# Optimization experiments

Measured on AMD Instinct MI355X. Metric: run time of the kernel, lower is better.

## Reference

```python
import jax, jax.numpy as jnp
import numpy as np

NUM_GRAPHS = 512


def setup_inputs() -> dict:
    key = jax.random.key(0)
    ks = jax.random.split(key, 12)
    N, F = 100000, 9
    E = 1600000
    x = jax.random.normal(ks[0], (N, F), dtype=jnp.float32)
    edge_index = jax.random.randint(ks[1], (2, E), 0, N, dtype=jnp.int64)
    batch = jnp.sort(jax.random.randint(ks[2], (N,), 0, NUM_GRAPHS, dtype=jnp.int64))
    def lin(k, fan_in, fan_out):
        k1, k2 = jax.random.split(k)
        bound = 1.0 / np.sqrt(fan_in)
        W = jax.random.uniform(k1, (fan_out, fan_in), jnp.float32, -bound, bound)
        b = jax.random.uniform(k2, (fan_out,), jnp.float32, -bound, bound)
        return W, b
    W1, b1 = lin(ks[3], F, 64)
    W2, b2 = lin(ks[4], 64, 128)
    W3, b3 = lin(ks[5], 128, 64)
    Wfc, bfc = lin(ks[6], 64, 11)
    return {"x": x, "edge_index": edge_index, "batch": batch,
            "W1": W1, "b1": b1, "W2": W2, "b2": b2,
            "W3": W3, "b3": b3, "Wfc": Wfc, "bfc": bfc}


def reference(x, edge_index, batch, W1, b1, W2, b2, W3, b3, Wfc, bfc):
    N = x.shape[0]
    src, dst = edge_index[0], edge_index[1]

    def gin_layer(h, W, b):
        # GINConv (eps=0): Lin((1+eps)*h_i + sum_{j->i} h_j), then relu
        agg = jax.ops.segment_sum(h[src], dst, num_segments=N)
        return jax.nn.relu((h + agg) @ W.T + b)

    h = gin_layer(x, W1, b1)   # [N, 64]
    h = gin_layer(h, W2, b2)   # [N, 128]
    h = gin_layer(h, W3, b3)   # [N, 64]

    # global_mean_pool over graph ids
    sums = jax.ops.segment_sum(h, batch, num_segments=NUM_GRAPHS)           # [G, 64]
    counts = jax.ops.segment_sum(jnp.ones((N,), h.dtype), batch,
                                 num_segments=NUM_GRAPHS)                   # [G]
    pooled = sums / jnp.maximum(counts, 1.0)[:, None]
    return pooled @ Wfc.T + bfc  # [G, num_classes]
```

## Files before the change

### kernel.cpp

```cpp
#include <hip/hip_runtime.h>
#include <hip/hip_bf16.h>


#define NBLK 256
#define CFBS 512
#define RB   128
#define NBMAX 1024
#define SCBS 1024

__device__ inline float bf2f(unsigned short u) {
    return __uint_as_float((unsigned)u << 16);
}
__device__ inline unsigned short f2bf(float f) {
    unsigned x = __float_as_uint(f);
    return (unsigned short)((x + 0x7FFFu + ((x >> 16) & 1u)) >> 16);
}
__device__ inline float lo16(unsigned u) { return __uint_as_float(u << 16); }
__device__ inline float hi16(unsigned u) { return __uint_as_float(u & 0xFFFF0000u); }


__global__ __launch_bounds__(CFBS) void count_kernel(
    const int* __restrict__ dst, int* __restrict__ cnt, int E, int NB)
{
    __shared__ int hist[NBMAX];
    int tid = threadIdx.x;
    for (int i = tid; i < NBMAX; i += CFBS) hist[i] = 0;
    __syncthreads();
    for (int e = blockIdx.x * CFBS + tid; e < E; e += NBLK * CFBS)
        atomicAdd(&hist[dst[e] >> 7], 1);
    __syncthreads();
    for (int b = tid; b < NB; b += CFBS)
        cnt[b * NBLK + blockIdx.x] = hist[b];
}

__global__ __launch_bounds__(SCBS) void scan_k1(
    const int* __restrict__ cnt, int* __restrict__ ofs,
    int* __restrict__ part, int NT)
{
    __shared__ int tmp[SCBS];
    int i = blockIdx.x * SCBS + threadIdx.x;
    int v = (i < NT) ? cnt[i] : 0;
    tmp[threadIdx.x] = v;
    __syncthreads();
    for (int off = 1; off < SCBS; off <<= 1) {
        int t = (threadIdx.x >= off) ? tmp[threadIdx.x - off] : 0;
        __syncthreads();
        tmp[threadIdx.x] += t;
        __syncthreads();
    }
    if (i < NT) ofs[i] = tmp[threadIdx.x] - v;
    if (threadIdx.x == SCBS - 1) part[blockIdx.x] = tmp[threadIdx.x];
}

__global__ __launch_bounds__(SCBS) void scan_k2(int* __restrict__ part, int B)
{
    __shared__ int tmp[SCBS];
    int v = (threadIdx.x < B) ? part[threadIdx.x] : 0;
    tmp[threadIdx.x] = v;
    __syncthreads();
    for (int off = 1; off < SCBS; off <<= 1) {
        int t = (threadIdx.x >= off) ? tmp[threadIdx.x - off] : 0;
        __syncthreads();
        tmp[threadIdx.x] += t;
        __syncthreads();
    }
    if (threadIdx.x < B) part[threadIdx.x] = tmp[threadIdx.x] - v;
}

__global__ __launch_bounds__(SCBS) void scan_k3(
    int* __restrict__ ofs, const int* __restrict__ part, int NT)
{
    int i = blockIdx.x * SCBS + threadIdx.x;
    if (i < NT) ofs[i] += part[blockIdx.x];
}

__global__ __launch_bounds__(CFBS) void fillp_kernel(
    const int* __restrict__ src, const int* __restrict__ dst,
    const int* __restrict__ ofs, int* __restrict__ pairs, int E, int NB)
{
    __shared__ int cur[NBMAX];
    int tid = threadIdx.x;
    for (int b = tid; b < NB; b += CFBS)
        cur[b] = ofs[b * NBLK + blockIdx.x];
    __syncthreads();
    for (int e = blockIdx.x * CFBS + tid; e < E; e += NBLK * CFBS) {
        int d = dst[e];
        int b = d >> 7, dl = d & 127;
        int pos = atomicAdd(&cur[b], 1);
        pairs[pos] = (dl << 20) | src[e];
    }
}

__global__ __launch_bounds__(512) void bucket_csr_kernel(
    const int* __restrict__ pairs, const int* __restrict__ ofs,
    int* __restrict__ rowstart, int* __restrict__ eidx, int N, int E, int NB)
{
    __shared__ int deg[RB], pfx[RB], cur[RB];
    int tid = threadIdx.x;
    int b = blockIdx.x, n0 = b << 7;
    int e0 = ofs[b * NBLK];
    int e1 = (b + 1 < NB) ? ofs[(b + 1) * NBLK] : E;
    if (tid < RB) deg[tid] = 0;
    __syncthreads();
    for (int e = e0 + tid; e < e1; e += 512)
        atomicAdd(&deg[pairs[e] >> 20], 1);
    __syncthreads();
    if (tid < RB) pfx[tid] = deg[tid];
    __syncthreads();
    for (int off = 1; off < RB; off <<= 1) {
        int t = (tid < RB && tid >= off) ? pfx[tid - off] : 0;
        __syncthreads();
        if (tid < RB) pfx[tid] += t;
        __syncthreads();
    }
    if (tid < RB) {
        int ex = pfx[tid] - deg[tid];
        cur[tid] = ex;
        int n = n0 + tid;
        if (n < N) rowstart[n] = e0 + ex;
    }
    if (b == NB - 1 && tid == 0) rowstart[N] = E;
    __syncthreads();
    for (int e = e0 + tid; e < e1; e += 512) {
        int p = pairs[e];
        int pos = e0 + atomicAdd(&cur[p >> 20], 1);
        eidx[pos] = p & 0xFFFFF;
    }
}


__global__ __launch_bounds__(256) void xprep_kernel(
    const float* __restrict__ x, unsigned short* __restrict__ xb, int N)
{
    int n = blockIdx.x * 256 + threadIdx.x;
    if (n >= N) return;
    unsigned short r[16];
    #pragma unroll
    for (int k = 0; k < 9; ++k) r[k] = f2bf(x[(size_t)n * 9 + k]);
    #pragma unroll
    for (int k = 9; k < 16; ++k) r[k] = 0;
    uint4 u0, u1;
    u0.x = r[0] | ((unsigned)r[1] << 16);  u0.y = r[2] | ((unsigned)r[3] << 16);
    u0.z = r[4] | ((unsigned)r[5] << 16);  u0.w = r[6] | ((unsigned)r[7] << 16);
    u1.x = r[8] | ((unsigned)r[9] << 16);  u1.y = 0; u1.z = 0; u1.w = 0;
    *(uint4*)&xb[(size_t)n * 16]     = u0;
    *(uint4*)&xb[(size_t)n * 16 + 8] = u1;
}


__global__ __launch_bounds__(256) void node1v_kernel(
    const unsigned short* __restrict__ xb, const int* __restrict__ rs,
    const int* __restrict__ eidx, const float* __restrict__ W1,
    const float* __restrict__ b1, unsigned short* __restrict__ h1, int N)
{
    __shared__ float Wl[576];
    __shared__ float bl[64];
    for (int i = threadIdx.x; i < 576; i += 256) Wl[i] = W1[i];
    if (threadIdx.x < 64) bl[threadIdx.x] = b1[threadIdx.x];
    __syncthreads();
    int wid = threadIdx.x >> 6;
    int lane = threadIdx.x & 63;
    int g  = lane >> 2;
    int d4 = lane & 3;
    int nb = blockIdx.x * 16 + wid * 4;
    if (nb >= N) return;

    int n[4], e0[4], dg[4];
    float A0[4], A1[4], A2[4], A3[4];
    #pragma unroll
    for (int i = 0; i < 4; ++i) {
        n[i] = min(nb + i, N - 1);
        e0[i] = rs[n[i]];
        dg[i] = rs[n[i] + 1] - e0[i];
        A0[i] = A1[i] = A2[i] = A3[i] = 0.f;
    }
    #pragma unroll
    for (int i = 0; i < 4; ++i) {
        if (g == 0) {
            uint2 u = *(const uint2*)&xb[(size_t)n[i] * 16 + d4 * 4];
            A0[i] += lo16(u.x); A1[i] += hi16(u.x);
            A2[i] += lo16(u.y); A3[i] += hi16(u.y);
        }
    }
    int mdeg = max(max(dg[0], dg[1]), max(dg[2], dg[3]));
    for (int w0 = 0; w0 < mdeg; w0 += 64) {
        int sidx[4], wd[4];
        #pragma unroll
        for (int i = 0; i < 4; ++i) {
            wd[i] = min(max(dg[i] - w0, 0), 64);
            sidx[i] = (lane < wd[i]) ? eidx[e0[i] + w0 + lane] : 0;
        }
        int mwd = max(max(wd[0], wd[1]), max(wd[2], wd[3]));
        for (int c = 0; c < mwd; c += 16) {
            #pragma unroll
            for (int i = 0; i < 4; ++i) {
                int idx = c + g;
                int s = __shfl(sidx[i], idx < wd[i] ? idx : 0);
                float m = (idx < wd[i]) ? 1.f : 0.f;
                uint2 u = *(const uint2*)&xb[(size_t)s * 16 + d4 * 4];
                A0[i] += m * lo16(u.x); A1[i] += m * hi16(u.x);
                A2[i] += m * lo16(u.y); A3[i] += m * hi16(u.y);
            }
        }
    }
    #pragma unroll
    for (int m = 4; m < 64; m <<= 1) {
        #pragma unroll
        for (int i = 0; i < 4; ++i) {
            A0[i] += __shfl_xor(A0[i], m); A1[i] += __shfl_xor(A1[i], m);
            A2[i] += __shfl_xor(A2[i], m); A3[i] += __shfl_xor(A3[i], m);
        }
    }
    const float* wr = &Wl[lane * 9];
    #pragma unroll
    for (int i = 0; i < 4; ++i) {
        float xv0 = __shfl(A0[i], 0), xv1 = __shfl(A1[i], 0);
        float xv2 = __shfl(A2[i], 0), xv3 = __shfl(A3[i], 0);
        float xv4 = __shfl(A0[i], 1), xv5 = __shfl(A1[i], 1);
        float xv6 = __shfl(A2[i], 1), xv7 = __shfl(A3[i], 1);
        float xv8 = __shfl(A0[i], 2);
        float s = bl[lane] + xv0 * wr[0] + xv1 * wr[1] + xv2 * wr[2]
                + xv3 * wr[3] + xv4 * wr[4] + xv5 * wr[5] + xv6 * wr[6]
                + xv7 * wr[7] + xv8 * wr[8];
        if (nb + i < N)
            h1[(size_t)(nb + i) * 64 + lane] = f2bf(fmaxf(s, 0.f));
    }
}


template<bool BIAS_RELU>
__global__ __launch_bounds__(256) void gather64v_kernel(
    const unsigned short* __restrict__ feat, const int* __restrict__ rs,
    const int* __restrict__ eidx, const float* __restrict__ bias,
    unsigned short* __restrict__ out, int N)
{
    int wid = threadIdx.x >> 6;
    int lane = threadIdx.x & 63;
    int g  = lane >> 4;
    int d4 = lane & 15;
    int nb = blockIdx.x * 16 + wid * 4;
    if (nb >= N) return;

    int n[4], e0[4], dg[4];
    float A0[4], A1[4], A2[4], A3[4];
    #pragma unroll
    for (int i = 0; i < 4; ++i) {
        n[i] = min(nb + i, N - 1);
        e0[i] = rs[n[i]];
        dg[i] = rs[n[i] + 1] - e0[i];
        A0[i] = A1[i] = A2[i] = A3[i] = 0.f;
    }
    #pragma unroll
    for (int i = 0; i < 4; ++i) {
        if (g == 0) {
            uint2 u = *(const uint2*)&feat[(size_t)n[i] * 64 + d4 * 4];
            A0[i] += lo16(u.x); A1[i] += hi16(u.x);
            A2[i] += lo16(u.y); A3[i] += hi16(u.y);
        }
    }
    int mdeg = max(max(dg[0], dg[1]), max(dg[2], dg[3]));
    for (int w0 = 0; w0 < mdeg; w0 += 64) {
        int sidx[4], wd[4];
        #pragma unroll
        for (int i = 0; i < 4; ++i) {
            wd[i] = min(max(dg[i] - w0, 0), 64);
            sidx[i] = (lane < wd[i]) ? eidx[e0[i] + w0 + lane] : 0;
        }
        int mwd = max(max(wd[0], wd[1]), max(wd[2], wd[3]));
        for (int c = 0; c < mwd; c += 8) {
            #pragma unroll
            for (int i = 0; i < 4; ++i) {
                int i0 = c + g, i1 = c + 4 + g;
                int s0 = __shfl(sidx[i], i0 < wd[i] ? i0 : 0);
                int s1 = __shfl(sidx[i], i1 < wd[i] ? i1 : 0);
                float m0 = (i0 < wd[i]) ? 1.f : 0.f;
                float m1 = (i1 < wd[i]) ? 1.f : 0.f;
                uint2 u0 = *(const uint2*)&feat[(size_t)s0 * 64 + d4 * 4];
                uint2 u1 = *(const uint2*)&feat[(size_t)s1 * 64 + d4 * 4];
                A0[i] += m0 * lo16(u0.x) + m1 * lo16(u1.x);
                A1[i] += m0 * hi16(u0.x) + m1 * hi16(u1.x);
                A2[i] += m0 * lo16(u0.y) + m1 * lo16(u1.y);
                A3[i] += m0 * hi16(u0.y) + m1 * hi16(u1.y);
            }
        }
    }
    #pragma unroll
    for (int m = 16; m < 64; m <<= 1) {
        #pragma unroll
        for (int i = 0; i < 4; ++i) {
            A0[i] += __shfl_xor(A0[i], m); A1[i] += __shfl_xor(A1[i], m);
            A2[i] += __shfl_xor(A2[i], m); A3[i] += __shfl_xor(A3[i], m);
        }
    }
    float4 bv = make_float4(0.f, 0.f, 0.f, 0.f);
    if (BIAS_RELU) bv = *(const float4*)&bias[d4 * 4];
    #pragma unroll
    for (int i = 0; i < 4; ++i) {
        if (g == 0 && nb + i < N) {
            float a0 = A0[i], a1 = A1[i], a2 = A2[i], a3 = A3[i];
            if (BIAS_RELU) {
                a0 = fmaxf(a0 + bv.x, 0.f); a1 = fmaxf(a1 + bv.y, 0.f);
                a2 = fmaxf(a2 + bv.z, 0.f); a3 = fmaxf(a3 + bv.w, 0.f);
            }
            ushort4 u;
            u.x = f2bf(a0); u.y = f2bf(a1); u.z = f2bf(a2); u.w = f2bf(a3);
            *(ushort4*)&out[(size_t)(nb + i) * 64 + d4 * 4] = u;
        }
    }
}


template<int IN, int OUT, bool RELU>
__global__ __launch_bounds__(256) void linear_mfma_kernel(
    const unsigned short* __restrict__ A, const float* __restrict__ W,
    const float* __restrict__ bias, unsigned short* __restrict__ Y, int N)
{
    using s8v = __attribute__((ext_vector_type(8))) short;
    using f4v = __attribute__((ext_vector_type(4))) float;
    constexpr int KT = IN / 32;
    constexpr int CT = OUT / 16;
    constexpr int INP = IN + 8;
    __shared__ __align__(16) unsigned short Wb[OUT * INP];
    __shared__ float bl[OUT];
    int tid = threadIdx.x;
    for (int i = tid; i < OUT * IN; i += 256) {
        int o = i / IN, k = i % IN;
        Wb[o * INP + k] = f2bf(W[i]);
    }
    for (int i = tid; i < OUT; i += 256) bl[i] = bias ? bias[i] : 0.f;
    __syncthreads();

    int w = tid >> 6, lane = tid & 63;
    int n0 = blockIdx.x * 64 + w * 16;
    int hl = lane >> 4;
    int ll = lane & 15;

    int an = n0 + ll;
    if (an >= N) an = N - 1;
    const unsigned short* arow = &A[(size_t)an * IN + hl * 8];
    s8v a[KT];
    #pragma unroll
    for (int ks = 0; ks < KT; ++ks) a[ks] = *(const s8v*)&arow[ks * 32];

    f4v acc[CT];
    #pragma unroll
    for (int c = 0; c < CT; ++c) acc[c] = (f4v){0.f, 0.f, 0.f, 0.f};
    #pragma unroll
    for (int c = 0; c < CT; ++c) {
        const unsigned short* wrow = &Wb[(c * 16 + ll) * INP + hl * 8];
        #pragma unroll
        for (int ks = 0; ks < KT; ++ks) {
            s8v b = *(const s8v*)&wrow[ks * 32];
            acc[c] = __builtin_amdgcn_mfma_f32_16x16x32_bf16(a[ks], b, acc[c], 0, 0, 0);
        }
    }
    #pragma unroll
    for (int c = 0; c < CT; ++c) {
        int col = c * 16 + ll;
        float bv = bl[col];
        #pragma unroll
        for (int r = 0; r < 4; ++r) {
            int gn = n0 + hl * 4 + r;
            if (gn < N) {
                float v = acc[c][r] + bv;
                if (RELU) v = fmaxf(v, 0.f);
                Y[(size_t)gn * OUT + col] = f2bf(v);
            }
        }
    }
}


__device__ inline int lower_bound_i(const int* a, int n, int v) {
    int lo = 0, hi = n;
    while (lo < hi) {
        int mid = (lo + hi) >> 1;
        if (a[mid] < v) lo = mid + 1; else hi = mid;
    }
    return lo;
}

__global__ __launch_bounds__(256) void pool_fc_kernel(
    const unsigned short* __restrict__ h3, const int* __restrict__ batch,
    const float* __restrict__ Wfc, const float* __restrict__ bfc,
    float* __restrict__ out, int N)
{
    int g = blockIdx.x;
    int tid = threadIdx.x;
    int w = tid >> 6, lane = tid & 63;
    int lo = lower_bound_i(batch, N, g);
    int hi = lower_bound_i(batch, N, g + 1);
    float sum = 0.f;
    for (int i = lo + w; i < hi; i += 4)
        sum += bf2f(h3[(size_t)i * 64 + lane]);
    __shared__ float P[4][64];
    P[w][lane] = sum;
    __syncthreads();
    if (w == 0) {
        float s = P[0][lane] + P[1][lane] + P[2][lane] + P[3][lane];
        float cnt = (float)((hi - lo) > 0 ? (hi - lo) : 1);
        P[0][lane] = s / cnt;
    }
    __syncthreads();
    if (tid < 11) {
        float s = bfc[tid];
        const float* wr = &Wfc[tid * 64];
        #pragma unroll 8
        for (int k = 0; k < 64; ++k) s += P[0][k] * wr[k];
        out[g * 11 + tid] = s;
    }
}


extern "C" void kernel_launch(void* const* d_in, const int* in_sizes, int n_in,
                              void* d_out, int out_size, void* d_ws, size_t ws_size,
                              hipStream_t stream) {
    const float* x    = (const float*)d_in[0];
    const int*   ei   = (const int*)d_in[1];
    const int*   batch= (const int*)d_in[2];
    const float* W1   = (const float*)d_in[3];
    const float* b1   = (const float*)d_in[4];
    const float* W2   = (const float*)d_in[5];
    const float* b2   = (const float*)d_in[6];
    const float* W3   = (const float*)d_in[7];
    const float* b3   = (const float*)d_in[8];
    const float* Wfc  = (const float*)d_in[9];
    const float* bfc  = (const float*)d_in[10];
    float* out = (float*)d_out;

    const int N = in_sizes[2];
    const int E = in_sizes[1] / 2;
    const int G = out_size / 11;
    const int* src = ei;
    const int* dst = ei + E;
    const int NB = (N + RB - 1) / RB;
    const int NT = NB * NBLK;
    const int SB = (NT + SCBS - 1) / SCBS;

    unsigned short* B1 = (unsigned short*)d_ws;
    unsigned short* B2 = B1 + (size_t)64 * N;
    unsigned short* B3 = B2 + (size_t)64 * N;
    unsigned short* XB = B3 + (size_t)128 * N;
    int* pairs    = (int*)(XB + (size_t)16 * N);
    int* eidx     = pairs + E;
    int* rowstart = eidx + E;
    int* cnt      = rowstart + (N + 1);
    int* ofs      = cnt + NT;
    int* part     = ofs + NT;

    unsigned short* h1   = B1;
    unsigned short* buf2 = B2;
    unsigned short* h2   = B3;
    unsigned short* t3   = B1;
    unsigned short* h3   = B2;
    unsigned short* xb   = XB;

    count_kernel<<<NBLK, CFBS, 0, stream>>>(dst, cnt, E, NB);
    scan_k1<<<SB, SCBS, 0, stream>>>(cnt, ofs, part, NT);
    scan_k2<<<1, SCBS, 0, stream>>>(part, SB);
    scan_k3<<<SB, SCBS, 0, stream>>>(ofs, part, NT);
    fillp_kernel<<<NBLK, CFBS, 0, stream>>>(src, dst, ofs, pairs, E, NB);
    bucket_csr_kernel<<<NB, 512, 0, stream>>>(pairs, ofs, rowstart, eidx, N, E, NB);
    xprep_kernel<<<(N + 255) / 256, 256, 0, stream>>>(x, xb, N);

    node1v_kernel<<<(N + 15) / 16, 256, 0, stream>>>(
        xb, rowstart, eidx, W1, b1, h1, N);

    gather64v_kernel<false><<<(N + 15) / 16, 256, 0, stream>>>(
        h1, rowstart, eidx, nullptr, buf2, N);
    linear_mfma_kernel<64, 128, true><<<(N + 63) / 64, 256, 0, stream>>>(
        buf2, W2, b2, h2, N);

    linear_mfma_kernel<128, 64, false><<<(N + 63) / 64, 256, 0, stream>>>(
        h2, W3, nullptr, t3, N);
    gather64v_kernel<true><<<(N + 15) / 16, 256, 0, stream>>>(
        t3, rowstart, eidx, b3, h3, N);

    pool_fc_kernel<<<G, 256, 0, stream>>>(h3, batch, Wfc, bfc, out, N);
}
```

Measured before the change: 209.6 us.

## Sort nodes by degree to balance per-wave gather work

Builds a degree histogram during CSR construction, scans it, and fills a permutation that groups nodes by in-degree (capped at 255). The three gather kernels process nodes in permuted order, so the four nodes sharing a wave have similar degrees and less time is lost waiting on the longest one. The cost is three extra small kernels plus a memset, an extra indirection per node, and scattered rather than contiguous output writes and self-feature reads. Degrees here are roughly Poisson around 16, so the imbalance being removed is modest.

```diff
diff --git a/kernel.cpp b/kernel.cpp
--- a/kernel.cpp
+++ b/kernel.cpp
@@ -93,7 +93,8 @@
 
 __global__ __launch_bounds__(512) void bucket_csr_kernel(
     const int* __restrict__ pairs, const int* __restrict__ ofs,
-    int* __restrict__ rowstart, int* __restrict__ eidx, int N, int E, int NB)
+    int* __restrict__ rowstart, int* __restrict__ eidx,
+    int* __restrict__ dcnt, int N, int E, int NB)
 {
     __shared__ int deg[RB], pfx[RB], cur[RB];
     int tid = threadIdx.x;
@@ -117,7 +118,10 @@
         int ex = pfx[tid] - deg[tid];
         cur[tid] = ex;
         int n = n0 + tid;
-        if (n < N) rowstart[n] = e0 + ex;
+        if (n < N) {
+            rowstart[n] = e0 + ex;
+            atomicAdd(&dcnt[min(deg[tid], 255)], 1);
+        }
     }
     if (b == NB - 1 && tid == 0) rowstart[N] = E;
     __syncthreads();
@@ -126,6 +130,33 @@
         int pos = e0 + atomicAdd(&cur[p >> 20], 1);
         eidx[pos] = p & 0xFFFFF;
     }
+}
+
+__global__ __launch_bounds__(256) void dscan_kernel(int* __restrict__ dcnt)
+{
+    __shared__ int tmp[256];
+    int i = threadIdx.x;
+    int v = dcnt[i];
+    tmp[i] = v;
+    __syncthreads();
+    for (int off = 1; off < 256; off <<= 1) {
+        int t = (i >= off) ? tmp[i - off] : 0;
+        __syncthreads();
+        tmp[i] += t;
+        __syncthreads();
+    }
+    dcnt[i] = tmp[i] - v;
+}
+
+__global__ __launch_bounds__(256) void dfill_kernel(
+    const int* __restrict__ rs, int* __restrict__ dcur,
+    int* __restrict__ perm, int N)
+{
+    int n = blockIdx.x * 256 + threadIdx.x;
+    if (n >= N) return;
+    int d = min(rs[n + 1] - rs[n], 255);
+    int pos = atomicAdd(&dcur[d], 1);
+    perm[pos] = n;
 }
 
 
@@ -150,8 +181,9 @@
 
 __global__ __launch_bounds__(256) void node1v_kernel(
     const unsigned short* __restrict__ xb, const int* __restrict__ rs,
-    const int* __restrict__ eidx, const float* __restrict__ W1,
-    const float* __restrict__ b1, unsigned short* __restrict__ h1, int N)
+    const int* __restrict__ eidx, const int* __restrict__ perm,
+    const float* __restrict__ W1, const float* __restrict__ b1,
+    unsigned short* __restrict__ h1, int N)
 {
     __shared__ float Wl[576];
     __shared__ float bl[64];
@@ -169,7 +201,7 @@
     float A0[4], A1[4], A2[4], A3[4];
     #pragma unroll
     for (int i = 0; i < 4; ++i) {
-        n[i] = min(nb + i, N - 1);
+        n[i] = perm[min(nb + i, N - 1)];
         e0[i] = rs[n[i]];
         dg[i] = rs[n[i] + 1] - e0[i];
         A0[i] = A1[i] = A2[i] = A3[i] = 0.f;
@@ -223,7 +255,7 @@
                 + xv3 * wr[3] + xv4 * wr[4] + xv5 * wr[5] + xv6 * wr[6]
                 + xv7 * wr[7] + xv8 * wr[8];
         if (nb + i < N)
-            h1[(size_t)(nb + i) * 64 + lane] = f2bf(fmaxf(s, 0.f));
+            h1[(size_t)n[i] * 64 + lane] = f2bf(fmaxf(s, 0.f));
     }
 }
 
@@ -231,8 +263,8 @@
 template<bool BIAS_RELU>
 __global__ __launch_bounds__(256) void gather64v_kernel(
     const unsigned short* __restrict__ feat, const int* __restrict__ rs,
-    const int* __restrict__ eidx, const float* __restrict__ bias,
-    unsigned short* __restrict__ out, int N)
+    const int* __restrict__ eidx, const int* __restrict__ perm,
+    const float* __restrict__ bias, unsigned short* __restrict__ out, int N)
 {
     int wid = threadIdx.x >> 6;
     int lane = threadIdx.x & 63;
@@ -245,7 +277,7 @@
     float A0[4], A1[4], A2[4], A3[4];
     #pragma unroll
     for (int i = 0; i < 4; ++i) {
-        n[i] = min(nb + i, N - 1);
+        n[i] = perm[min(nb + i, N - 1)];
         e0[i] = rs[n[i]];
         dg[i] = rs[n[i] + 1] - e0[i];
         A0[i] = A1[i] = A2[i] = A3[i] = 0.f;
@@ -304,7 +336,7 @@
             }
             ushort4 u;
             u.x = f2bf(a0); u.y = f2bf(a1); u.z = f2bf(a2); u.w = f2bf(a3);
-            *(ushort4*)&out[(size_t)(nb + i) * 64 + d4 * 4] = u;
+            *(ushort4*)&out[(size_t)n[i] * 64 + d4 * 4] = u;
         }
     }
 }
@@ -444,7 +476,9 @@
     int* pairs    = (int*)(XB + (size_t)16 * N);
     int* eidx     = pairs + E;
     int* rowstart = eidx + E;
-    int* cnt      = rowstart + (N + 1);
+    int* perm     = rowstart + (N + 1);
+    int* dcnt     = perm + N;
+    int* cnt      = dcnt + 256;
     int* ofs      = cnt + NT;
     int* part     = ofs + NT;
 
@@ -460,21 +494,24 @@
     scan_k2<<<1, SCBS, 0, stream>>>(part, SB);
     scan_k3<<<SB, SCBS, 0, stream>>>(ofs, part, NT);
     fillp_kernel<<<NBLK, CFBS, 0, stream>>>(src, dst, ofs, pairs, E, NB);
-    bucket_csr_kernel<<<NB, 512, 0, stream>>>(pairs, ofs, rowstart, eidx, N, E, NB);
+    hipMemsetAsync(dcnt, 0, 256 * sizeof(int), stream);
+    bucket_csr_kernel<<<NB, 512, 0, stream>>>(pairs, ofs, rowstart, eidx, dcnt, N, E, NB);
+    dscan_kernel<<<1, 256, 0, stream>>>(dcnt);
+    dfill_kernel<<<(N + 255) / 256, 256, 0, stream>>>(rowstart, dcnt, perm, N);
     xprep_kernel<<<(N + 255) / 256, 256, 0, stream>>>(x, xb, N);
 
     node1v_kernel<<<(N + 15) / 16, 256, 0, stream>>>(
-        xb, rowstart, eidx, W1, b1, h1, N);
+        xb, rowstart, eidx, perm, W1, b1, h1, N);
 
     gather64v_kernel<false><<<(N + 15) / 16, 256, 0, stream>>>(
-        h1, rowstart, eidx, nullptr, buf2, N);
+        h1, rowstart, eidx, perm, nullptr, buf2, N);
     linear_mfma_kernel<64, 128, true><<<(N + 63) / 64, 256, 0, stream>>>(
         buf2, W2, b2, h2, N);
 
     linear_mfma_kernel<128, 64, false><<<(N + 63) / 64, 256, 0, stream>>>(
         h2, W3, nullptr, t3, N);
     gather64v_kernel<true><<<(N + 15) / 16, 256, 0, stream>>>(
-        t3, rowstart, eidx, b3, h3, N);
+        t3, rowstart, eidx, perm, b3, h3, N);
 
     pool_fc_kernel<<<G, 256, 0, stream>>>(h3, batch, Wfc, bfc, out, N);
 }
```

Result: slower. 762.2 us (+263.6%).

## Fuse layer-2 and layer-3 linear MFMA kernels and unroll gather loop deeper

Applied to the files above, without the earlier changes.

Merges the two back-to-back linear kernels into one. The 128-wide relu'd hidden activation now stays in LDS and feeds the second MFMA product directly, so it is never written to and re-read from global memory. It also widens the neighbor-gather inner loop from 8 to 16 neighbors per step, putting more independent loads in flight. The costs are more LDS per block (two weight tiles plus an activation tile), which may lower occupancy, higher register pressure in the gather, and more wasted masked loads for low-degree nodes.

```diff
diff --git a/kernel.cpp b/kernel.cpp
--- a/kernel.cpp
+++ b/kernel.cpp
@@ -267,20 +267,31 @@
             sidx[i] = (lane < wd[i]) ? eidx[e0[i] + w0 + lane] : 0;
         }
         int mwd = max(max(wd[0], wd[1]), max(wd[2], wd[3]));
-        for (int c = 0; c < mwd; c += 8) {
+        for (int c = 0; c < mwd; c += 16) {
             #pragma unroll
             for (int i = 0; i < 4; ++i) {
                 int i0 = c + g, i1 = c + 4 + g;
+                int i2 = c + 8 + g, i3 = c + 12 + g;
                 int s0 = __shfl(sidx[i], i0 < wd[i] ? i0 : 0);
                 int s1 = __shfl(sidx[i], i1 < wd[i] ? i1 : 0);
+                int s2 = __shfl(sidx[i], i2 < wd[i] ? i2 : 0);
+                int s3 = __shfl(sidx[i], i3 < wd[i] ? i3 : 0);
                 float m0 = (i0 < wd[i]) ? 1.f : 0.f;
                 float m1 = (i1 < wd[i]) ? 1.f : 0.f;
+                float m2 = (i2 < wd[i]) ? 1.f : 0.f;
+                float m3 = (i3 < wd[i]) ? 1.f : 0.f;
                 uint2 u0 = *(const uint2*)&feat[(size_t)s0 * 64 + d4 * 4];
                 uint2 u1 = *(const uint2*)&feat[(size_t)s1 * 64 + d4 * 4];
-                A0[i] += m0 * lo16(u0.x) + m1 * lo16(u1.x);
-                A1[i] += m0 * hi16(u0.x) + m1 * hi16(u1.x);
-                A2[i] += m0 * lo16(u0.y) + m1 * lo16(u1.y);
-                A3[i] += m0 * hi16(u0.y) + m1 * hi16(u1.y);
+                uint2 u2 = *(const uint2*)&feat[(size_t)s2 * 64 + d4 * 4];
+                uint2 u3 = *(const uint2*)&feat[(size_t)s3 * 64 + d4 * 4];
+                A0[i] += (m0 * lo16(u0.x) + m1 * lo16(u1.x))
+                       + (m2 * lo16(u2.x) + m3 * lo16(u3.x));
+                A1[i] += (m0 * hi16(u0.x) + m1 * hi16(u1.x))
+                       + (m2 * hi16(u2.x) + m3 * hi16(u3.x));
+                A2[i] += (m0 * lo16(u0.y) + m1 * lo16(u1.y))
+                       + (m2 * lo16(u2.y) + m3 * lo16(u3.y));
+                A3[i] += (m0 * hi16(u0.y) + m1 * hi16(u1.y))
+                       + (m2 * hi16(u2.y) + m3 * hi16(u3.y));
             }
         }
     }
@@ -310,24 +321,27 @@
 }
 
 
-template<int IN, int OUT, bool RELU>
-__global__ __launch_bounds__(256) void linear_mfma_kernel(
-    const unsigned short* __restrict__ A, const float* __restrict__ W,
-    const float* __restrict__ bias, unsigned short* __restrict__ Y, int N)
+__global__ __launch_bounds__(256) void linear23_fused_kernel(
+    const unsigned short* __restrict__ A, const float* __restrict__ W2,
+    const float* __restrict__ b2, const float* __restrict__ W3,
+    unsigned short* __restrict__ t3, int N)
 {
     using s8v = __attribute__((ext_vector_type(8))) short;
     using f4v = __attribute__((ext_vector_type(4))) float;
-    constexpr int KT = IN / 32;
-    constexpr int CT = OUT / 16;
-    constexpr int INP = IN + 8;
-    __shared__ __align__(16) unsigned short Wb[OUT * INP];
-    __shared__ float bl[OUT];
+    __shared__ __align__(16) unsigned short Wb2[128 * 72];
+    __shared__ __align__(16) unsigned short Wb3[64 * 136];
+    __shared__ __align__(16) unsigned short H2[64 * 136];
+    __shared__ float bl2[128];
     int tid = threadIdx.x;
-    for (int i = tid; i < OUT * IN; i += 256) {
-        int o = i / IN, k = i % IN;
-        Wb[o * INP + k] = f2bf(W[i]);
-    }
-    for (int i = tid; i < OUT; i += 256) bl[i] = bias ? bias[i] : 0.f;
+    for (int i = tid; i < 128 * 64; i += 256) {
+        int o = i >> 6, k = i & 63;
+        Wb2[o * 72 + k] = f2bf(W2[i]);
+    }
+    for (int i = tid; i < 64 * 128; i += 256) {
+        int o = i >> 7, k = i & 127;
+        Wb3[o * 136 + k] = f2bf(W3[i]);
+    }
+    if (tid < 128) bl2[tid] = b2[tid];
     __syncthreads();
 
     int w = tid >> 6, lane = tid & 63;
@@ -335,37 +349,45 @@
     int hl = lane >> 4;
     int ll = lane & 15;
 
-    int an = n0 + ll;
-    if (an >= N) an = N - 1;
-    const unsigned short* arow = &A[(size_t)an * IN + hl * 8];
-    s8v a[KT];
-    #pragma unroll
-    for (int ks = 0; ks < KT; ++ks) a[ks] = *(const s8v*)&arow[ks * 32];
-
-    f4v acc[CT];
-    #pragma unroll
-    for (int c = 0; c < CT; ++c) acc[c] = (f4v){0.f, 0.f, 0.f, 0.f};
-    #pragma unroll
-    for (int c = 0; c < CT; ++c) {
-        const unsigned short* wrow = &Wb[(c * 16 + ll) * INP + hl * 8];
-        #pragma unroll
-        for (int ks = 0; ks < KT; ++ks) {
-            s8v b = *(const s8v*)&wrow[ks * 32];
-            acc[c] = __builtin_amdgcn_mfma_f32_16x16x32_bf16(a[ks], b, acc[c], 0, 0, 0);
-        }
-    }
-    #pragma unroll
-    for (int c = 0; c < CT; ++c) {
+    int an = min(n0 + ll, N - 1);
+    const unsigned short* arow = &A[(size_t)an * 64 + hl * 8];
+    s8v a1[2];
+    a1[0] = *(const s8v*)&arow[0];
+    a1[1] = *(const s8v*)&arow[32];
+
+    #pragma unroll
+    for (int c = 0; c < 8; ++c) {
+        f4v acc = (f4v){0.f, 0.f, 0.f, 0.f};
+        const unsigned short* wrow = &Wb2[(c * 16 + ll) * 72 + hl * 8];
+        acc = __builtin_amdgcn_mfma_f32_16x16x32_bf16(a1[0], *(const s8v*)&wrow[0],  acc, 0, 0, 0);
+        acc = __builtin_amdgcn_mfma_f32_16x16x32_bf16(a1[1], *(const s8v*)&wrow[32], acc, 0, 0, 0);
         int col = c * 16 + ll;
-        float bv = bl[col];
+        float bv = bl2[col];
+        #pragma unroll
+        for (int r = 0; r < 4; ++r) {
+            int nrow = w * 16 + hl * 4 + r;
+            H2[nrow * 136 + col] = f2bf(fmaxf(acc[r] + bv, 0.f));
+        }
+    }
+
+    const unsigned short* hrow = &H2[(w * 16 + ll) * 136 + hl * 8];
+    s8v a2[4];
+    #pragma unroll
+    for (int ks = 0; ks < 4; ++ks) a2[ks] = *(const s8v*)&hrow[ks * 32];
+
+    #pragma unroll
+    for (int c = 0; c < 4; ++c) {
+        f4v acc = (f4v){0.f, 0.f, 0.f, 0.f};
+        const unsigned short* wrow = &Wb3[(c * 16 + ll) * 136 + hl * 8];
+        #pragma unroll
+        for (int ks = 0; ks < 4; ++ks)
+            acc = __builtin_amdgcn_mfma_f32_16x16x32_bf16(a2[ks], *(const s8v*)&wrow[ks * 32], acc, 0, 0, 0);
+        int col = c * 16 + ll;
         #pragma unroll
         for (int r = 0; r < 4; ++r) {
             int gn = n0 + hl * 4 + r;
-            if (gn < N) {
-                float v = acc[c][r] + bv;
-                if (RELU) v = fmaxf(v, 0.f);
-                Y[(size_t)gn * OUT + col] = f2bf(v);
-            }
+            if (gn < N)
+                t3[(size_t)gn * 64 + col] = f2bf(acc[r]);
         }
     }
 }
@@ -439,8 +461,7 @@
 
     unsigned short* B1 = (unsigned short*)d_ws;
     unsigned short* B2 = B1 + (size_t)64 * N;
-    unsigned short* B3 = B2 + (size_t)64 * N;
-    unsigned short* XB = B3 + (size_t)128 * N;
+    unsigned short* XB = B2 + (size_t)64 * N;
     int* pairs    = (int*)(XB + (size_t)16 * N);
     int* eidx     = pairs + E;
     int* rowstart = eidx + E;
@@ -450,7 +471,6 @@
 
     unsigned short* h1   = B1;
     unsigned short* buf2 = B2;
-    unsigned short* h2   = B3;
     unsigned short* t3   = B1;
     unsigned short* h3   = B2;
     unsigned short* xb   = XB;
@@ -468,11 +488,9 @@
 
     gather64v_kernel<false><<<(N + 15) / 16, 256, 0, stream>>>(
         h1, rowstart, eidx, nullptr, buf2, N);
-    linear_mfma_kernel<64, 128, true><<<(N + 63) / 64, 256, 0, stream>>>(
-        buf2, W2, b2, h2, N);
-
-    linear_mfma_kernel<128, 64, false><<<(N + 63) / 64, 256, 0, stream>>>(
-        h2, W3, nullptr, t3, N);
+    linear23_fused_kernel<<<(N + 63) / 64, 256, 0, stream>>>(
+        buf2, W2, b2, W3, t3, N);
+
     gather64v_kernel<true><<<(N + 15) / 16, 256, 0, stream>>>(
         t3, rowstart, eidx, b3, h3, N);
 
```

New measurement: 223.2 us. 6.5% more time.
